# Kernel tuning notes

Hardware: AMD Instinct MI355X
Metric: run time of the kernel (lower is better)

The kernel has to match this reference:

```python
import jax, jax.numpy as jnp
import numpy as np

B, N, DIM = 4, 4096, 1024
HEADS, DIM_HEAD = 16, 64
DIM_INNER = HEADS * DIM_HEAD
ATTN_SCALE = 8.0
EPS = 1e-12  # F.normalize default eps


def setup_inputs() -> dict:
    key = jax.random.key(0)
    k1, k2, k3, k4, k5 = jax.random.split(key, 5)
    x = jax.random.normal(k1, (B, N, DIM), dtype=jnp.float32)
    gamma = jnp.ones((DIM,), dtype=jnp.float32)
    # stored as (in, out) so forward is x @ w
    w_qkv = jax.random.normal(k2, (DIM, 3 * DIM_INNER), dtype=jnp.float32) * (DIM ** -0.5)
    temperature = jnp.ones((HEADS, 1, 1), dtype=jnp.float32)
    w_out = jax.random.normal(k3, (DIM_INNER, DIM), dtype=jnp.float32) * (DIM_INNER ** -0.5)
    return {"x": x, "gamma": gamma, "w_qkv": w_qkv, "temperature": temperature, "w_out": w_out}


def _l2norm(t):
    # F.normalize(t, dim=-1): t / max(||t||_2, eps)
    n = jnp.linalg.norm(t, axis=-1, keepdims=True)
    return t / jnp.maximum(n, EPS)


def reference(x, gamma, w_qkv, temperature, w_out):
    b, n, dim = x.shape
    # RMSNorm: F.normalize(x, dim=-1) * sqrt(dim) * gamma
    xn = _l2norm(x) * (dim ** 0.5) * gamma
    # QKV projection -> qkv b h d n
    qkv = (xn @ w_qkv).reshape(b, n, 3, HEADS, DIM_HEAD)
    qkv = qkv.transpose(2, 0, 3, 4, 1)  # (3, b, h, d, n)
    q, k, v = qkv[0], qkv[1], qkv[2]
    # l2-normalize q, k over the sequence (last) axis; temperature-scale q
    q = _l2norm(q) * jnp.exp(temperature)  # temperature: (h,1,1) broadcast
    k = _l2norm(k)
    # cross-covariance attention over the small channel dim d
    sim = jnp.einsum('bhdn,bhen->bhde', q, k) * ATTN_SCALE
    attn = jax.nn.softmax(sim, axis=-1)
    out = jnp.einsum('bhde,bhen->bhdn', attn, v)
    # b h d n -> b n (h d), then out projection
    out = out.transpose(0, 3, 1, 2).reshape(b, n, DIM_INNER)
    return out @ w_out
```

## Files before the change

kernel.cpp:

```cpp
#include <hip/hip_runtime.h>
#include <stdint.h>

typedef unsigned short u16;
typedef unsigned int u32;
typedef __attribute__((ext_vector_type(8))) __bf16 bf16x8;
typedef __attribute__((ext_vector_type(4))) float f32x4;

#define M_TOT 16384
#define DIMX  1024

__device__ __forceinline__ u16 f2b(float f) {
  u32 u = __builtin_bit_cast(u32, f);
  u32 r = (u + 0x7fffu + ((u >> 16) & 1u)) >> 16;
  return (u16)r;
}

__device__ __forceinline__ void gl2lds16(const void* g, void* l) {
  __builtin_amdgcn_global_load_lds((const __attribute__((address_space(1))) void*)g,
                                   (__attribute__((address_space(3))) void*)l,
                                   16, 0, 0);
}

__global__ __launch_bounds__(256) void k_rms(const float* __restrict__ x,
                                             const float* __restrict__ gamma,
                                             u16* __restrict__ xn) {
  int row = blockIdx.x;
  int t = threadIdx.x;
  const float4* xr = (const float4*)(x + (size_t)row * DIMX);
  float4 v = xr[t];
  float ss = v.x * v.x + v.y * v.y + v.z * v.z + v.w * v.w;
#pragma unroll
  for (int o = 32; o > 0; o >>= 1) ss += __shfl_xor(ss, o, 64);
  __shared__ float wss[4];
  int w = t >> 6;
  if ((t & 63) == 0) wss[w] = ss;
  __syncthreads();
  float tot = wss[0] + wss[1] + wss[2] + wss[3];
  float scale = 32.0f / fmaxf(sqrtf(tot), 1e-12f);
  float4 g = ((const float4*)gamma)[t];
  ushort4 o4;
  o4.x = f2b(v.x * scale * g.x);
  o4.y = f2b(v.y * scale * g.y);
  o4.z = f2b(v.z * scale * g.z);
  o4.w = f2b(v.w * scale * g.w);
  ((ushort4*)xn)[(size_t)row * 256 + t] = o4;
}

__global__ __launch_bounds__(256) void k_castT(const float* __restrict__ in,
                                               u16* __restrict__ out, int Rr, int Cc) {
  __shared__ float tile[32][33];
  int c0 = blockIdx.x * 32, r0 = blockIdx.y * 32;
  int tx = threadIdx.x, ty = threadIdx.y;
#pragma unroll
  for (int i = 0; i < 4; i++)
    tile[ty + i * 8][tx] = in[(size_t)(r0 + ty + i * 8) * Cc + c0 + tx];
  __syncthreads();
#pragma unroll
  for (int i = 0; i < 4; i++)
    out[(size_t)(c0 + ty + i * 8) * Rr + r0 + tx] = f2b(tile[tx][ty + i * 8]);
}

template<bool SWAP>
__device__ __forceinline__ void gemm_core128(const u16* __restrict__ Ag,
                                             const u16* __restrict__ Bg,
                                             u16* Al, u16* Bl,
                                             int t, f32x4 (&acc)[4][4]) {
  int w = t >> 6, lane = t & 63;
  int r16 = lane & 15, q = lane >> 4;
  int wi = w >> 1, wj = w & 1;
  int swz = (r16 >> 1) & 3;
  int qs8 = ((q ^ swz) & 3) * 8;
  for (int k0 = 0; k0 < 1024; k0 += 64) {
    __syncthreads();
#pragma unroll
    for (int h = 0; h < 2; h++) {
#pragma unroll
      for (int r = 0; r < 2; r++) {
        int chunk = (r << 8) + t;
        int row = chunk >> 2;
        int cc = (chunk & 3) ^ ((row >> 1) & 3);
        u16* la = Al + h * 4096 + ((r << 8) + (w << 6)) * 8;
        u16* lb = Bl + h * 4096 + ((r << 8) + (w << 6)) * 8;
        gl2lds16(Ag + (size_t)row * 1024 + k0 + h * 32 + cc * 8, la);
        gl2lds16(Bg + (size_t)row * 1024 + k0 + h * 32 + cc * 8, lb);
      }
    }
    __syncthreads();
#pragma unroll
    for (int h = 0; h < 2; h++) {
      bf16x8 af[4], bfr[4];
#pragma unroll
      for (int i = 0; i < 4; i++) {
        af[i]  = *(const bf16x8*)(Al + h * 4096 + (wi * 64 + i * 16 + r16) * 32 + qs8);
        bfr[i] = *(const bf16x8*)(Bl + h * 4096 + (wj * 64 + i * 16 + r16) * 32 + qs8);
      }
#pragma unroll
      for (int i = 0; i < 4; i++)
#pragma unroll
        for (int j = 0; j < 4; j++)
          acc[i][j] = SWAP
            ? __builtin_amdgcn_mfma_f32_16x16x32_bf16(bfr[j], af[i], acc[i][j], 0, 0, 0)
            : __builtin_amdgcn_mfma_f32_16x16x32_bf16(af[i], bfr[j], acc[i][j], 0, 0, 0);
    }
  }
}

__global__ __launch_bounds__(256) void k_gemm1(const u16* __restrict__ A,
                                               const u16* __restrict__ Bt,
                                               u16* __restrict__ qkT,
                                               u16* __restrict__ vmat,
                                               float* __restrict__ sumsq) {
  __shared__ u16 Al[2 * 4096];
  __shared__ u16 Bl[2 * 4096];
  int l = blockIdx.x;
  int xcd = l & 7, idx = l >> 3;
  int m0 = (xcd * 16 + (idx & 15)) * 128;
  int n0 = (idx >> 4) * 128;
  int t = threadIdx.x, lane = t & 63, w = t >> 6;
  int wi = w >> 1, wj = w & 1;
  int r16 = lane & 15, q = lane >> 4;
  f32x4 acc[4][4] = {};
  if (n0 < 2048) {
    gemm_core128<false>(A + (size_t)m0 * 1024, Bt + (size_t)n0 * 1024, Al, Bl, t, acc);
    int b = m0 >> 12;
#pragma unroll
    for (int j = 0; j < 4; j++) {
      int c = n0 + wj * 64 + j * 16 + r16;
      float colss = 0.f;
#pragma unroll
      for (int i = 0; i < 4; i++) {
        f32x4 a = acc[i][j];
        colss += a.x * a.x + a.y * a.y + a.z * a.z + a.w * a.w;
        int m = m0 + wi * 64 + i * 16 + q * 4;
        ushort4 o4;
        o4.x = f2b(a.x); o4.y = f2b(a.y); o4.z = f2b(a.z); o4.w = f2b(a.w);
        *(ushort4*)(qkT + (size_t)c * M_TOT + m) = o4;
      }
      colss += __shfl_xor(colss, 16, 64);
      colss += __shfl_xor(colss, 32, 64);
      if (lane < 16) atomicAdd(&sumsq[b * 2048 + c], colss);
    }
  } else {
    gemm_core128<true>(A + (size_t)m0 * 1024, Bt + (size_t)n0 * 1024, Al, Bl, t, acc);
    int vc0 = n0 - 2048;
#pragma unroll
    for (int i = 0; i < 4; i++) {
      int m = m0 + wi * 64 + i * 16 + r16;
#pragma unroll
      for (int j = 0; j < 4; j++) {
        int c = vc0 + wj * 64 + j * 16 + q * 4;
        f32x4 a = acc[i][j];
        ushort4 o4;
        o4.x = f2b(a.x); o4.y = f2b(a.y); o4.z = f2b(a.z); o4.w = f2b(a.w);
        *(ushort4*)(vmat + (size_t)m * 1024 + c) = o4;
      }
    }
  }
}

__global__ __launch_bounds__(256) void k_attn_s(const u16* __restrict__ qkT,
                                                float* __restrict__ S) {
  int bh = blockIdx.x, split = blockIdx.y;
  int b = bh >> 4, h = bh & 15;
  int t = threadIdx.x, lane = t & 63, w = t >> 6;
  int r16 = lane & 15, q = lane >> 4;
  const u16* qbase = qkT + (size_t)(h * 64) * M_TOT + b * 4096;
  const u16* kbase = qkT + (size_t)(1024 + h * 64) * M_TOT + b * 4096;
  f32x4 acc[4][4] = {};
#pragma unroll
  for (int it = 0; it < 4; it++) {
    int n0 = split * 512 + it * 128 + w * 32;
    int kk = n0 + q * 8;
    bf16x8 af[4], bfr[4];
#pragma unroll
    for (int i = 0; i < 4; i++) af[i] = *(const bf16x8*)(qbase + (size_t)(i * 16 + r16) * M_TOT + kk);
#pragma unroll
    for (int j = 0; j < 4; j++) bfr[j] = *(const bf16x8*)(kbase + (size_t)(j * 16 + r16) * M_TOT + kk);
#pragma unroll
    for (int i = 0; i < 4; i++)
#pragma unroll
      for (int j = 0; j < 4; j++)
        acc[i][j] = __builtin_amdgcn_mfma_f32_16x16x32_bf16(af[i], bfr[j], acc[i][j], 0, 0, 0);
  }
  float* Sb = S + (size_t)bh * 4096;
#pragma unroll
  for (int i = 0; i < 4; i++) {
    int d0 = i * 16 + q * 4;
#pragma unroll
    for (int j = 0; j < 4; j++) {
      int e = j * 16 + r16;
      atomicAdd(&Sb[(d0 + 0) * 64 + e], acc[i][j].x);
      atomicAdd(&Sb[(d0 + 1) * 64 + e], acc[i][j].y);
      atomicAdd(&Sb[(d0 + 2) * 64 + e], acc[i][j].z);
      atomicAdd(&Sb[(d0 + 3) * 64 + e], acc[i][j].w);
    }
  }
}

__global__ __launch_bounds__(64) void k_softmax(const float* __restrict__ S,
                                                const float* __restrict__ sumsq,
                                                const float* __restrict__ temp,
                                                u16* __restrict__ PT) {
  int bh = blockIdx.x;
  int b = bh >> 4, h = bh & 15;
  int d = threadIdx.x;
  __shared__ float rnk[64];
  rnk[d] = 1.0f / fmaxf(sqrtf(sumsq[b * 2048 + 1024 + h * 64 + d]), 1e-12f);
  __syncthreads();
  float nq = sqrtf(sumsq[b * 2048 + h * 64 + d]);
  float qs = 8.0f * __expf(temp[h]) / fmaxf(nq, 1e-12f);
  const float* Srow = S + ((size_t)bh * 64 + d) * 64;
  float vals[64];
  float mx = -3.0e38f;
#pragma unroll
  for (int e = 0; e < 64; e++) {
    float v = Srow[e] * qs * rnk[e];
    vals[e] = v;
    mx = fmaxf(mx, v);
  }
  float sum = 0.f;
#pragma unroll
  for (int e = 0; e < 64; e++) {
    float v = __expf(vals[e] - mx);
    vals[e] = v;
    sum += v;
  }
  float inv = 1.0f / sum;
#pragma unroll
  for (int e = 0; e < 64; e++)
    PT[((size_t)bh * 64 + e) * 64 + d] = f2b(vals[e] * inv);
}

__global__ __launch_bounds__(256) void k_m(const u16* __restrict__ woT,
                                           const u16* __restrict__ PT,
                                           u16* __restrict__ MT) {
  int bh = blockIdx.x;
  int b = bh >> 4, h = bh & 15;
  int o0 = blockIdx.y * 128;
  int t = threadIdx.x, lane = t & 63, w = t >> 6;
  int r16 = lane & 15, q = lane >> 4;
  const u16* pbase = PT + (size_t)bh * 4096;
  f32x4 acc[2][4] = {};
#pragma unroll
  for (int ks = 0; ks < 2; ks++) {
    int kk = ks * 32 + q * 8;
    bf16x8 af[2], bfr[4];
#pragma unroll
    for (int i = 0; i < 2; i++)
      af[i] = *(const bf16x8*)(woT + (size_t)(o0 + w * 32 + i * 16 + r16) * 1024 + h * 64 + kk);
#pragma unroll
    for (int j = 0; j < 4; j++)
      bfr[j] = *(const bf16x8*)(pbase + (size_t)(j * 16 + r16) * 64 + kk);
#pragma unroll
    for (int i = 0; i < 2; i++)
#pragma unroll
      for (int j = 0; j < 4; j++)
        acc[i][j] = __builtin_amdgcn_mfma_f32_16x16x32_bf16(af[i], bfr[j], acc[i][j], 0, 0, 0);
  }
  u16* dst = MT + (size_t)b * 1024 * 1024;
#pragma unroll
  for (int i = 0; i < 2; i++) {
    int o = o0 + w * 32 + i * 16 + q * 4;
#pragma unroll
    for (int j = 0; j < 4; j++) {
      int e = h * 64 + j * 16 + r16;
      f32x4 a = acc[i][j];
      dst[(size_t)(o + 0) * 1024 + e] = f2b(a.x);
      dst[(size_t)(o + 1) * 1024 + e] = f2b(a.y);
      dst[(size_t)(o + 2) * 1024 + e] = f2b(a.z);
      dst[(size_t)(o + 3) * 1024 + e] = f2b(a.w);
    }
  }
}

__global__ __launch_bounds__(256) void k_gemm2(const u16* __restrict__ A,
                                               const u16* __restrict__ Bt,
                                               float* __restrict__ C) {
  __shared__ u16 Al[2 * 4096];
  __shared__ u16 Bl[2 * 4096];
  int l = blockIdx.x;
  int xcd = l & 7, idx = l >> 3;
  int m0 = (xcd * 16 + (idx & 15)) * 128;
  int n0 = (idx >> 4) * 128;
  int b = m0 >> 12;
  const u16* Bb = Bt + (size_t)b * 1024 * 1024;
  int t = threadIdx.x, lane = t & 63, w = t >> 6;
  int wi = w >> 1, wj = w & 1;
  int r16 = lane & 15, q = lane >> 4;
  f32x4 acc[4][4] = {};
  gemm_core128<true>(A + (size_t)m0 * 1024, Bb + (size_t)n0 * 1024, Al, Bl, t, acc);
#pragma unroll
  for (int i = 0; i < 4; i++) {
    int m = m0 + wi * 64 + i * 16 + r16;
#pragma unroll
    for (int j = 0; j < 4; j++) {
      int c = n0 + wj * 64 + j * 16 + q * 4;
      *(f32x4*)(C + (size_t)m * 1024 + c) = acc[i][j];
    }
  }
}

extern "C" void kernel_launch(void* const* d_in, const int* in_sizes, int n_in,
                              void* d_out, int out_size, void* d_ws, size_t ws_size,
                              hipStream_t stream) {
  const float* x     = (const float*)d_in[0];
  const float* gamma = (const float*)d_in[1];
  const float* wqkv  = (const float*)d_in[2];
  const float* temp  = (const float*)d_in[3];
  const float* wout  = (const float*)d_in[4];
  float* out = (float*)d_out;

  char* ws = (char*)d_ws;
  size_t off = 0;
  u16* xn = (u16*)(ws + off);    off += (size_t)M_TOT * 1024 * 2;
  u16* wqT = (u16*)(ws + off);   off += (size_t)3072 * 1024 * 2;
  u16* woT = (u16*)(ws + off);   off += (size_t)1024 * 1024 * 2;
  u16* qkT = (u16*)(ws + off);   off += (size_t)2048 * M_TOT * 2;
  u16* vmat = (u16*)(ws + off);  off += (size_t)M_TOT * 1024 * 2;
  float* sumsq = (float*)(ws + off); off += (size_t)4 * 2048 * 4;
  float* S = (float*)(ws + off); off += (size_t)64 * 64 * 64 * 4;
  u16* PT = (u16*)(ws + off);    off += (size_t)64 * 64 * 64 * 2;
  u16* MT = (u16*)(ws + off);    off += (size_t)4 * 1024 * 1024 * 2;

  hipMemsetAsync((void*)sumsq, 0, (size_t)4 * 2048 * 4 + (size_t)64 * 64 * 64 * 4, stream);

  k_rms<<<16384, 256, 0, stream>>>(x, gamma, xn);
  dim3 cb(32, 8);
  k_castT<<<dim3(3072 / 32, 1024 / 32), cb, 0, stream>>>(wqkv, wqT, 1024, 3072);
  k_castT<<<dim3(1024 / 32, 1024 / 32), cb, 0, stream>>>(wout, woT, 1024, 1024);
  k_gemm1<<<3072, 256, 0, stream>>>(xn, wqT, qkT, vmat, sumsq);
  k_attn_s<<<dim3(64, 8), 256, 0, stream>>>(qkT, S);
  k_softmax<<<64, 64, 0, stream>>>(S, sumsq, temp, PT);
  k_m<<<dim3(64, 8), 256, 0, stream>>>(woT, PT, MT);
  k_gemm2<<<1024, 256, 0, stream>>>(vmat, MT, out);
}
```

Baseline: 375.2 us.

## Replace atomic S accumulation with per-split partial buffers reduced in softmax

The Gram-matrix kernel stops accumulating split-K partials with global float atomics. Each wave now owns one (batch, head) and writes its partial S tile with vectorized stores into a per-split buffer, and the softmax kernel sums the 16 partials. The partial buffer reuses the xn workspace, which is dead after gemm1, and the memset of S is dropped. The cost is extra memory traffic for 16 partial tiles and a reduction loop in the single-wave softmax blocks.

```diff
diff --git a/kernel.cpp b/kernel.cpp
--- a/kernel.cpp
+++ b/kernel.cpp
@@ -159,18 +159,18 @@
 }
 
 __global__ __launch_bounds__(256) void k_attn_s(const u16* __restrict__ qkT,
-                                                float* __restrict__ S) {
-  int bh = blockIdx.x, split = blockIdx.y;
+                                                float* __restrict__ Spart) {
+  int g = blockIdx.x, split = blockIdx.y;
+  int t = threadIdx.x, lane = t & 63, w = t >> 6;
+  int bh = g * 4 + w;
   int b = bh >> 4, h = bh & 15;
-  int t = threadIdx.x, lane = t & 63, w = t >> 6;
   int r16 = lane & 15, q = lane >> 4;
   const u16* qbase = qkT + (size_t)(h * 64) * M_TOT + b * 4096;
   const u16* kbase = qkT + (size_t)(1024 + h * 64) * M_TOT + b * 4096;
   f32x4 acc[4][4] = {};
 #pragma unroll
-  for (int it = 0; it < 4; it++) {
-    int n0 = split * 512 + it * 128 + w * 32;
-    int kk = n0 + q * 8;
+  for (int it = 0; it < 8; it++) {
+    int kk = split * 256 + it * 32 + q * 8;
     bf16x8 af[4], bfr[4];
 #pragma unroll
     for (int i = 0; i < 4; i++) af[i] = *(const bf16x8*)(qbase + (size_t)(i * 16 + r16) * M_TOT + kk);
@@ -180,24 +180,21 @@
     for (int i = 0; i < 4; i++)
 #pragma unroll
       for (int j = 0; j < 4; j++)
-        acc[i][j] = __builtin_amdgcn_mfma_f32_16x16x32_bf16(af[i], bfr[j], acc[i][j], 0, 0, 0);
-  }
-  float* Sb = S + (size_t)bh * 4096;
+        acc[i][j] = __builtin_amdgcn_mfma_f32_16x16x32_bf16(bfr[j], af[i], acc[i][j], 0, 0, 0);
+  }
+  float* Sp = Spart + ((size_t)split * 64 + bh) * 4096;
 #pragma unroll
   for (int i = 0; i < 4; i++) {
-    int d0 = i * 16 + q * 4;
+    int d = i * 16 + r16;
 #pragma unroll
     for (int j = 0; j < 4; j++) {
-      int e = j * 16 + r16;
-      atomicAdd(&Sb[(d0 + 0) * 64 + e], acc[i][j].x);
-      atomicAdd(&Sb[(d0 + 1) * 64 + e], acc[i][j].y);
-      atomicAdd(&Sb[(d0 + 2) * 64 + e], acc[i][j].z);
-      atomicAdd(&Sb[(d0 + 3) * 64 + e], acc[i][j].w);
-    }
-  }
-}
-
-__global__ __launch_bounds__(64) void k_softmax(const float* __restrict__ S,
+      int e = j * 16 + q * 4;
+      *(f32x4*)(Sp + d * 64 + e) = acc[i][j];
+    }
+  }
+}
+
+__global__ __launch_bounds__(64) void k_softmax(const float* __restrict__ Spart,
                                                 const float* __restrict__ sumsq,
                                                 const float* __restrict__ temp,
                                                 u16* __restrict__ PT) {
@@ -209,12 +206,20 @@
   __syncthreads();
   float nq = sqrtf(sumsq[b * 2048 + h * 64 + d]);
   float qs = 8.0f * __expf(temp[h]) / fmaxf(nq, 1e-12f);
-  const float* Srow = S + ((size_t)bh * 64 + d) * 64;
+  const float* Sp = Spart + (size_t)bh * 4096 + d * 64;
   float vals[64];
+#pragma unroll
+  for (int e = 0; e < 64; e += 4) {
+    f32x4 v = {};
+#pragma unroll
+    for (int s = 0; s < 16; s++)
+      v += *(const f32x4*)(Sp + (size_t)s * 64 * 4096 + e);
+    vals[e + 0] = v.x; vals[e + 1] = v.y; vals[e + 2] = v.z; vals[e + 3] = v.w;
+  }
   float mx = -3.0e38f;
 #pragma unroll
   for (int e = 0; e < 64; e++) {
-    float v = Srow[e] * qs * rnk[e];
+    float v = vals[e] * qs * rnk[e];
     vals[e] = v;
     mx = fmaxf(mx, v);
   }
@@ -318,19 +323,20 @@
   u16* qkT = (u16*)(ws + off);   off += (size_t)2048 * M_TOT * 2;
   u16* vmat = (u16*)(ws + off);  off += (size_t)M_TOT * 1024 * 2;
   float* sumsq = (float*)(ws + off); off += (size_t)4 * 2048 * 4;
-  float* S = (float*)(ws + off); off += (size_t)64 * 64 * 64 * 4;
   u16* PT = (u16*)(ws + off);    off += (size_t)64 * 64 * 64 * 2;
   u16* MT = (u16*)(ws + off);    off += (size_t)4 * 1024 * 1024 * 2;
 
-  hipMemsetAsync((void*)sumsq, 0, (size_t)4 * 2048 * 4 + (size_t)64 * 64 * 64 * 4, stream);
+  float* Spart = (float*)xn;
+
+  hipMemsetAsync((void*)sumsq, 0, (size_t)4 * 2048 * 4, stream);
 
   k_rms<<<16384, 256, 0, stream>>>(x, gamma, xn);
   dim3 cb(32, 8);
   k_castT<<<dim3(3072 / 32, 1024 / 32), cb, 0, stream>>>(wqkv, wqT, 1024, 3072);
   k_castT<<<dim3(1024 / 32, 1024 / 32), cb, 0, stream>>>(wout, woT, 1024, 1024);
   k_gemm1<<<3072, 256, 0, stream>>>(xn, wqT, qkT, vmat, sumsq);
-  k_attn_s<<<dim3(64, 8), 256, 0, stream>>>(qkT, S);
-  k_softmax<<<64, 64, 0, stream>>>(S, sumsq, temp, PT);
+  k_attn_s<<<dim3(16, 16), 256, 0, stream>>>(qkT, Spart);
+  k_softmax<<<64, 64, 0, stream>>>(Spart, sumsq, temp, PT);
   k_m<<<dim3(64, 8), 256, 0, stream>>>(woT, PT, MT);
   k_gemm2<<<1024, 256, 0, stream>>>(vmat, MT, out);
 }
```

After: 367.2 us. -2.1%, faster.
